# Performance work log

Measured on AMD Instinct MI355X. Metric: run time of the kernel, lower is better.

The kernel has to match this reference:

```python
import jax, jax.numpy as jnp
import numpy as np

C = 256
G = 32            # GroupNorm groups = min(32, C)
DQK = C // 8      # q/k channel dim
EPS = 1e-5


def setup_inputs() -> dict:
    key = jax.random.key(0)
    ks = jax.random.split(key, 10)
    B, H, W = 4, 64, 64
    s = 0.02
    return {
        "x": jax.random.normal(ks[0], (B, C, H, W), dtype=jnp.float32),
        "gamma": jnp.ones((C,), jnp.float32),
        "beta": jnp.zeros((C,), jnp.float32),
        "wq": jax.random.normal(ks[1], (DQK, C), jnp.float32) * s,
        "bq": jnp.zeros((DQK,), jnp.float32),
        "wk": jax.random.normal(ks[2], (DQK, C), jnp.float32) * s,
        "bk": jnp.zeros((DQK,), jnp.float32),
        "wv": jax.random.normal(ks[3], (C, C), jnp.float32) * s,
        "bv": jnp.zeros((C,), jnp.float32),
        "wp": jax.random.normal(ks[4], (C, C), jnp.float32) * s,
        "bp": jnpp if False else jnp.zeros((C,), jnp.float32),
    }


def reference(x, gamma, beta, wq, bq, wk, bk, wv, bv, wp, bp):
    B, Cc, H, W = x.shape
    N = H * W
    # GroupNorm(32, C), affine
    h = x.reshape(B, G, Cc // G, H, W)
    mu = h.mean(axis=(2, 3, 4), keepdims=True)
    var = h.var(axis=(2, 3, 4), keepdims=True)
    h = (h - mu) * jax.lax.rsqrt(var + EPS)
    h = h.reshape(B, Cc, N) * gamma[:, None] + beta[:, None]
    # 1x1 convs == per-token linear maps over channels
    q = jnp.einsum('dc,bcn->bnd', wq, h) + bq            # [B, N, DQK]
    k = jnp.einsum('dc,bcn->bdn', wk, h) + bk[:, None]   # [B, DQK, N]
    v = jnp.einsum('ec,bcn->ben', wv, h) + bv[:, None]   # [B, C, N]
    scale = DQK ** (-0.5)
    attn = jax.nn.softmax(jnp.einsum('bnd,bdm->bnm', q, k) * scale, axis=-1)
    out = jnp.einsum('bnm,bem->ben', attn, v)            # [B, C, N]
    proj = jnp.einsum('fe,ben->bfn', wp, out) + bp[:, None]
    return x + proj.reshape(B, Cc, H, W)
```

## Files before the change

### kernel.cpp

```cpp
#include <hip/hip_runtime.h>
#include <hip/hip_bf16.h>

#define NB 4
#define CD 256
#define NT 4096
#define DQ 32

typedef __attribute__((ext_vector_type(8))) __bf16 bf16x8;
typedef __attribute__((ext_vector_type(16))) float float16v;
typedef __attribute__((ext_vector_type(4))) unsigned int uint4v;
typedef __attribute__((ext_vector_type(2))) unsigned int uint2v;

#if __has_builtin(__builtin_amdgcn_exp2f)
#define EXP2(x) __builtin_amdgcn_exp2f(x)
#else
#define EXP2(x) exp2f(x)
#endif

__device__ inline unsigned short f2bf(float f) {
  unsigned u = __float_as_uint(f);
  u += 0x7fffu + ((u >> 16) & 1u);
  return (unsigned short)(u >> 16);
}

__global__ __launch_bounds__(256) void gn_prep(
    const float* __restrict__ x, float* __restrict__ accum,
    const float* __restrict__ wq, const float* __restrict__ wk,
    const float* __restrict__ wv, const float* __restrict__ wp,
    const float* __restrict__ bq, const float* __restrict__ bk,
    const float* __restrict__ bv, unsigned short* __restrict__ wqkv,
    unsigned short* __restrict__ wpb, float* __restrict__ bias) {
  int bx = blockIdx.x;
  int tid = threadIdx.x;
  if (bx < 512) {
    int bg = bx >> 2, ch = bx & 3;
    const float4* xp = (const float4*)(x + (size_t)bg * 32768 + ch * 8192);
    float s = 0.f, ss = 0.f;
#pragma unroll
    for (int i = 0; i < 8; i++) {
      float4 v = xp[tid + 256 * i];
      s += v.x + v.y + v.z + v.w;
      ss += v.x * v.x + v.y * v.y + v.z * v.z + v.w * v.w;
    }
    int wid = tid >> 6, lane = tid & 63;
#pragma unroll
    for (int off = 32; off >= 1; off >>= 1) {
      s += __shfl_xor(s, off);
      ss += __shfl_xor(ss, off);
    }
    __shared__ float red[8];
    if (lane == 0) { red[wid] = s; red[4 + wid] = ss; }
    __syncthreads();
    if (tid == 0) {
      accum[2 * bx] = red[0] + red[1] + red[2] + red[3];
      accum[2 * bx + 1] = red[4] + red[5] + red[6] + red[7];
    }
  } else {
    const float scale2 = 0.2550348909867343f;
    int i = (bx - 512) * 256 + tid;
    if (i < 320 * 256) {
      int j = i >> 8, c = i & 255;
      float v;
      if (j < 32) v = wq[j * 256 + c] * scale2;
      else if (j < 64) v = wk[(j - 32) * 256 + c];
      else v = wv[(j - 64) * 256 + c];
      wqkv[i] = f2bf(v);
    } else if (i < 320 * 256 + 256 * 256) {
      int k = i - 320 * 256;
      wpb[k] = f2bf(wp[k]);
    } else if (i < 320 * 256 + 256 * 256 + 320) {
      int j = i - (320 * 256 + 256 * 256);
      float v;
      if (j < 32) v = bq[j] * scale2;
      else if (j < 64) v = bk[j - 32];
      else v = bv[j - 64];
      bias[j] = v;
    }
  }
}

__global__ __launch_bounds__(256) void gn_apply(
    const float* __restrict__ x, const float* __restrict__ gamma,
    const float* __restrict__ beta, const float* __restrict__ accum,
    unsigned short* __restrict__ h) {
  int bg = blockIdx.x >> 2, nc = blockIdx.x & 3;
  int tid = threadIdx.x;
  float S = accum[8 * bg] + accum[8 * bg + 2] + accum[8 * bg + 4] +
            accum[8 * bg + 6];
  float SS = accum[8 * bg + 1] + accum[8 * bg + 3] + accum[8 * bg + 5] +
             accum[8 * bg + 7];
  float mu = S * (1.f / 32768.f);
  float var = SS * (1.f / 32768.f) - mu * mu;
  float rstd = rsqrtf(var + 1e-5f);
  int b = bg >> 5, g = bg & 31, c0 = g * 8;
  float gam[8], bet[8];
#pragma unroll
  for (int j = 0; j < 8; j++) { gam[j] = gamma[c0 + j]; bet[j] = beta[c0 + j]; }
  const float* xb = x + (size_t)bg * 32768;
#pragma unroll
  for (int i = 0; i < 4; i++) {
    int n = nc * 1024 + tid + 256 * i;
    unsigned short hv[8];
#pragma unroll
    for (int j = 0; j < 8; j++) {
      float y = (xb[j * NT + n] - mu) * rstd * gam[j] + bet[j];
      hv[j] = f2bf(y);
    }
    *(uint4v*)(h + ((size_t)(b * NT + n) * CD + c0)) = *(uint4v*)hv;
  }
}

__global__ __launch_bounds__(256) void qkv_gemm(
    const unsigned short* __restrict__ A, const unsigned short* __restrict__ H,
    const float* __restrict__ bias, unsigned short* __restrict__ qk,
    unsigned short* __restrict__ v) {
  int nt = blockIdx.x, mt = blockIdx.y, b = blockIdx.z;
  int tid = threadIdx.x, lane = tid & 63;
  int w = tid >> 6, mi = w & 1, ni = w >> 1;
  int l31 = lane & 31, hh = lane >> 5;
  int m_base = mt * 64 + 32 * mi;
  int n_base = nt * 128 + 64 * ni;
  const unsigned short* Arow = A + (size_t)(m_base + l31) * 256 + 8 * hh;
  const unsigned short* Hb = H + (size_t)b * NT * CD;
  const unsigned short* h0 = Hb + (size_t)(n_base + l31) * CD + 8 * hh;
  const unsigned short* h1 = h0 + (size_t)32 * CD;
  float16v acc0, acc1;
#pragma unroll
  for (int r = 0; r < 16; r++) { acc0[r] = 0.f; acc1[r] = 0.f; }
#pragma unroll
  for (int s = 0; s < 16; s++) {
    bf16x8 af = *(const bf16x8*)(Arow + 16 * s);
    bf16x8 b0 = *(const bf16x8*)(h0 + 16 * s);
    bf16x8 b1 = *(const bf16x8*)(h1 + 16 * s);
    acc0 = __builtin_amdgcn_mfma_f32_32x32x16_bf16(af, b0, acc0, 0, 0, 0);
    acc1 = __builtin_amdgcn_mfma_f32_32x32x16_bf16(af, b1, acc1, 0, 0, 0);
  }
  float bj[16];
  int jr[16];
#pragma unroll
  for (int r = 0; r < 16; r++) {
    jr[r] = m_base + (r & 3) + 8 * (r >> 2) + 4 * hh;
    bj[r] = bias[jr[r]];
  }
#pragma unroll
  for (int half = 0; half < 2; half++) {
    int n = n_base + 32 * half + l31;
#pragma unroll
    for (int r = 0; r < 16; r++) {
      float val = (half ? acc1[r] : acc0[r]) + bj[r];
      int j = jr[r];
      if (j < 64) {
        qk[((size_t)b * NT + n) * 64 + j] = f2bf(val);
      } else {
        v[((size_t)b * CD + (j - 64)) * NT + n] = f2bf(val);
      }
    }
  }
}

__global__ __launch_bounds__(512, 4) void attn_fused(
    const unsigned short* __restrict__ qk, const unsigned short* __restrict__ V,
    unsigned short* __restrict__ Pa, unsigned short* __restrict__ Pb,
    float* __restrict__ lp4) {
  int bx = blockIdx.x;
  int n0 = (bx >> 1) * 64;
  int kh = bx & 1;
  int b = blockIdx.y;
  int tid = threadIdx.x, lane = tid & 63, w = tid >> 6;
  int qi = w & 1, kj = (w >> 1) & 1, eo = w >> 2;
  int l31 = lane & 31, hh = lane >> 5;

  __shared__ unsigned short Ks[64 * 36];
  __shared__ unsigned short Vs[256 * 68];
  __shared__ unsigned short Pbuf[2 * 32 * 68];

  const unsigned short* qkb = qk + (size_t)b * NT * 64;
  const unsigned short* Vb = V + (size_t)b * CD * NT;

  int n_g = n0 + 32 * qi + l31;
  bf16x8 qfr[2];
  qfr[0] = *(const bf16x8*)&qkb[(size_t)n_g * 64 + 8 * hh];
  qfr[1] = *(const bf16x8*)&qkb[(size_t)n_g * 64 + 8 * hh + 16];

  int se = tid >> 1, smh = (tid & 1) * 32;
  int skr = tid >> 2, skc = (tid & 3) * 8;

  int mbase = kh * 2048;
  uint4v vreg[4];
  uint4v kreg;
  {
    const unsigned short* vp = &Vb[(size_t)se * NT + mbase + smh];
#pragma unroll
    for (int u = 0; u < 4; u++) vreg[u] = *(const uint4v*)(vp + 8 * u);
    if (tid < 256)
      kreg = *(const uint4v*)&qkb[(size_t)(mbase + skr) * 64 + 32 + skc];
  }

  float16v acc[2];
#pragma unroll
  for (int et = 0; et < 2; et++)
#pragma unroll
    for (int r = 0; r < 16; r++) acc[et][r] = 0.f;
  float lsum = 0.f;
  unsigned short* Prow = &Pbuf[(qi * 32 + l31) * 68];

  for (int it = 0; it < 32; it++) {
    if (tid < 256) {
      *(uint4v*)&Ks[skr * 36 + skc] = kreg;
      if (it + 1 < 32) {
        int m1 = mbase + (it + 1) * 64;
        kreg = *(const uint4v*)&qkb[(size_t)(m1 + skr) * 64 + 32 + skc];
      }
    }
    __syncthreads();

#pragma unroll
    for (int u = 0; u < 4; u++)
      *(uint4v*)&Vs[se * 68 + smh + 8 * u] = vreg[u];
    if (it + 1 < 32) {
      int m1 = mbase + (it + 1) * 64;
      const unsigned short* vp = &Vb[(size_t)se * NT + m1 + smh];
#pragma unroll
      for (int u = 0; u < 4; u++) vreg[u] = *(const uint4v*)(vp + 8 * u);
    }

    if (eo == 0) {
      float16v st;
#pragma unroll
      for (int r = 0; r < 16; r++) st[r] = 0.f;
#pragma unroll
      for (int s = 0; s < 2; s++) {
        bf16x8 af = *(const bf16x8*)&Ks[(32 * kj + l31) * 36 + 16 * s + 8 * hh];
        st = __builtin_amdgcn_mfma_f32_32x32x16_bf16(af, qfr[s], st, 0, 0, 0);
      }
#pragma unroll
      for (int rq = 0; rq < 4; rq++) {
        float e0 = EXP2(st[4 * rq + 0]);
        float e1 = EXP2(st[4 * rq + 1]);
        float e2 = EXP2(st[4 * rq + 2]);
        float e3 = EXP2(st[4 * rq + 3]);
        lsum += (e0 + e1) + (e2 + e3);
        uint2v pw;
        pw[0] = __builtin_amdgcn_perm(__float_as_uint(e1), __float_as_uint(e0),
                                      0x07060302u);
        pw[1] = __builtin_amdgcn_perm(__float_as_uint(e3), __float_as_uint(e2),
                                      0x07060302u);
        *(uint2v*)&Prow[8 * rq + 4 * hh + 32 * kj] = pw;
      }
    }
    __syncthreads();

#pragma unroll
    for (int sp = 0; sp < 4; sp++) {
      bf16x8 afr =
          *(const bf16x8*)&Pbuf[(qi * 32 + l31) * 68 + 16 * sp + 8 * hh];
#pragma unroll
      for (int et = 0; et < 2; et++) {
        int etile = 4 * eo + 2 * kj + et;
        bf16x8 bfr =
            *(const bf16x8*)&Vs[(32 * etile + l31) * 68 + 16 * sp + 8 * hh];
        acc[et] =
            __builtin_amdgcn_mfma_f32_32x32x16_bf16(afr, bfr, acc[et], 0, 0, 0);
      }
    }
  }

  if (eo == 0) {
    lsum += __shfl_xor(lsum, 32);
    if (hh == 0) {
      lp4[(size_t)((kh * 2 + kj) * NB + b) * NT + n0 + 32 * qi + l31] = lsum;
    }
  }
  unsigned short* Pout = (kh ? Pb : Pa) + (size_t)b * NT * CD;
#pragma unroll
  for (int r = 0; r < 16; r++) {
    int nl = (r & 3) + 8 * (r >> 2) + 4 * hh;
    size_t row = (size_t)(n0 + 32 * qi + nl) * CD + l31;
#pragma unroll
    for (int et = 0; et < 2; et++) {
      int etile = 4 * eo + 2 * kj + et;
      Pout[row + 32 * etile] = f2bf(acc[et][r]);
    }
  }
}

__device__ inline bf16x8 combine_frag(const unsigned short* p0,
                                      const unsigned short* p1, float inv) {
  uint4v ua = *(const uint4v*)p0;
  uint4v ub = *(const uint4v*)p1;
  uint4v r;
#pragma unroll
  for (int j = 0; j < 4; j++) {
    float lo = __uint_as_float(ua[j] << 16) + __uint_as_float(ub[j] << 16);
    float hi = __uint_as_float(ua[j] & 0xffff0000u) +
               __uint_as_float(ub[j] & 0xffff0000u);
    lo *= inv;
    hi *= inv;
    r[j] = __builtin_amdgcn_perm(__float_as_uint(hi), __float_as_uint(lo),
                                 0x07060302u);
  }
  return *(bf16x8*)&r;
}

__global__ __launch_bounds__(256) void proj_gemm(
    const unsigned short* __restrict__ Wp, const unsigned short* __restrict__ Pa,
    const unsigned short* __restrict__ Pb, const float* __restrict__ lp4,
    const float* __restrict__ bp, const float* __restrict__ x,
    float* __restrict__ out) {
  int nt = blockIdx.x, mt = blockIdx.y, b = blockIdx.z;
  int tid = threadIdx.x, lane = tid & 63;
  int w = tid >> 6, mi = w & 1, ni = w >> 1;
  int l31 = lane & 31, hh = lane >> 5;
  int m_base = mt * 64 + 32 * mi;
  int n_base = nt * 128 + 64 * ni;
  const unsigned short* Arow = Wp + (size_t)(m_base + l31) * 256 + 8 * hh;
  int nA = n_base + l31, nB = nA + 32;
  float lA = 0.f, lB = 0.f;
#pragma unroll
  for (int s4 = 0; s4 < 4; s4++) {
    lA += lp4[(size_t)(s4 * NB + b) * NT + nA];
    lB += lp4[(size_t)(s4 * NB + b) * NT + nB];
  }
  float invA = 1.f / lA, invB = 1.f / lB;
  const unsigned short* a0 = Pa + ((size_t)b * NT + nA) * CD + 8 * hh;
  const unsigned short* a1 = Pa + ((size_t)b * NT + nB) * CD + 8 * hh;
  const unsigned short* c0 = Pb + ((size_t)b * NT + nA) * CD + 8 * hh;
  const unsigned short* c1 = Pb + ((size_t)b * NT + nB) * CD + 8 * hh;
  float16v acc0, acc1;
#pragma unroll
  for (int r = 0; r < 16; r++) { acc0[r] = 0.f; acc1[r] = 0.f; }
#pragma unroll
  for (int s = 0; s < 16; s++) {
    bf16x8 af = *(const bf16x8*)(Arow + 16 * s);
    bf16x8 b0 = combine_frag(a0 + 16 * s, c0 + 16 * s, invA);
    bf16x8 b1 = combine_frag(a1 + 16 * s, c1 + 16 * s, invB);
    acc0 = __builtin_amdgcn_mfma_f32_32x32x16_bf16(af, b0, acc0, 0, 0, 0);
    acc1 = __builtin_amdgcn_mfma_f32_32x32x16_bf16(af, b1, acc1, 0, 0, 0);
  }
#pragma unroll
  for (int half = 0; half < 2; half++) {
    int n = n_base + 32 * half + l31;
#pragma unroll
    for (int r = 0; r < 16; r++) {
      int f = m_base + (r & 3) + 8 * (r >> 2) + 4 * hh;
      size_t idx = ((size_t)b * CD + f) * NT + n;
      out[idx] = x[idx] + (half ? acc1[r] : acc0[r]) + bp[f];
    }
  }
}

extern "C" void kernel_launch(void* const* d_in, const int* in_sizes, int n_in,
                              void* d_out, int out_size, void* d_ws,
                              size_t ws_size, hipStream_t stream) {
  (void)in_sizes; (void)n_in; (void)out_size; (void)ws_size;
  const float* x = (const float*)d_in[0];
  const float* gamma = (const float*)d_in[1];
  const float* beta = (const float*)d_in[2];
  const float* wq = (const float*)d_in[3];
  const float* bq = (const float*)d_in[4];
  const float* wk = (const float*)d_in[5];
  const float* bk = (const float*)d_in[6];
  const float* wv = (const float*)d_in[7];
  const float* bv = (const float*)d_in[8];
  const float* wp = (const float*)d_in[9];
  const float* bp = (const float*)d_in[10];
  float* out = (float*)d_out;

  char* ws = (char*)d_ws;
  unsigned short* h_ws = (unsigned short*)ws;
  unsigned short* qk_ws = (unsigned short*)(ws + 8388608);
  unsigned short* v_ws = (unsigned short*)(ws + 10485760);
  unsigned short* o_ws = (unsigned short*)(ws + 18874368);
  unsigned short* wqkv_b = (unsigned short*)(ws + 27262976);
  unsigned short* wp_b = (unsigned short*)(ws + 27426816);
  float* bias_q = (float*)(ws + 27557888);
  float* accum = (float*)(ws + 27559168);
  float* lp4 = (float*)(ws + 27563264);

  gn_prep<<<1090, 256, 0, stream>>>(x, accum, wq, wk, wv, wp, bq, bk, bv,
                                    wqkv_b, wp_b, bias_q);
  gn_apply<<<512, 256, 0, stream>>>(x, gamma, beta, accum, h_ws);
  dim3 gq(32, 5, NB);
  qkv_gemm<<<gq, 256, 0, stream>>>(wqkv_b, h_ws, bias_q, qk_ws, v_ws);
  dim3 ga(128, NB);
  attn_fused<<<ga, 512, 0, stream>>>(qk_ws, v_ws, h_ws, o_ws, lp4);
  dim3 gp(32, 4, NB);
  proj_gemm<<<gp, 256, 0, stream>>>(wp_b, h_ws, o_ws, lp4, bp, x, out);
}
```

Before: 192.4 us.

## Fuse GroupNorm kernels and widen attention query tile to 128 rows

```diff
diff --git a/kernel.cpp b/kernel.cpp
--- a/kernel.cpp
+++ b/kernel.cpp
@@ -23,22 +23,23 @@
   return (unsigned short)(u >> 16);
 }
 
-__global__ __launch_bounds__(256) void gn_prep(
-    const float* __restrict__ x, float* __restrict__ accum,
-    const float* __restrict__ wq, const float* __restrict__ wk,
-    const float* __restrict__ wv, const float* __restrict__ wp,
-    const float* __restrict__ bq, const float* __restrict__ bk,
-    const float* __restrict__ bv, unsigned short* __restrict__ wqkv,
+__global__ __launch_bounds__(512) void gn_pack(
+    const float* __restrict__ x, const float* __restrict__ gamma,
+    const float* __restrict__ beta, const float* __restrict__ wq,
+    const float* __restrict__ wk, const float* __restrict__ wv,
+    const float* __restrict__ wp, const float* __restrict__ bq,
+    const float* __restrict__ bk, const float* __restrict__ bv,
+    unsigned short* __restrict__ h, unsigned short* __restrict__ wqkv,
     unsigned short* __restrict__ wpb, float* __restrict__ bias) {
   int bx = blockIdx.x;
   int tid = threadIdx.x;
-  if (bx < 512) {
-    int bg = bx >> 2, ch = bx & 3;
-    const float4* xp = (const float4*)(x + (size_t)bg * 32768 + ch * 8192);
+  if (bx < 128) {
+    int bg = bx;
+    const float4* xp = (const float4*)(x + (size_t)bg * 32768);
     float s = 0.f, ss = 0.f;
 #pragma unroll
-    for (int i = 0; i < 8; i++) {
-      float4 v = xp[tid + 256 * i];
+    for (int i = 0; i < 16; i++) {
+      float4 v = xp[tid + 512 * i];
       s += v.x + v.y + v.z + v.w;
       ss += v.x * v.x + v.y * v.y + v.z * v.z + v.w * v.w;
     }
@@ -48,16 +49,43 @@
       s += __shfl_xor(s, off);
       ss += __shfl_xor(ss, off);
     }
-    __shared__ float red[8];
-    if (lane == 0) { red[wid] = s; red[4 + wid] = ss; }
+    __shared__ float red[16];
+    __shared__ float stat[2];
+    if (lane == 0) { red[wid] = s; red[8 + wid] = ss; }
     __syncthreads();
     if (tid == 0) {
-      accum[2 * bx] = red[0] + red[1] + red[2] + red[3];
-      accum[2 * bx + 1] = red[4] + red[5] + red[6] + red[7];
+      float S = 0.f, SS = 0.f;
+#pragma unroll
+      for (int j = 0; j < 8; j++) { S += red[j]; SS += red[8 + j]; }
+      float mu = S * (1.f / 32768.f);
+      float var = SS * (1.f / 32768.f) - mu * mu;
+      stat[0] = mu;
+      stat[1] = rsqrtf(var + 1e-5f);
+    }
+    __syncthreads();
+    float mu = stat[0], rstd = stat[1];
+    int b = bg >> 5, g = bg & 31, c0 = g * 8;
+    float gam[8], bet[8];
+#pragma unroll
+    for (int j = 0; j < 8; j++) {
+      gam[j] = gamma[c0 + j];
+      bet[j] = beta[c0 + j];
+    }
+    const float* xb = x + (size_t)bg * 32768;
+#pragma unroll
+    for (int i = 0; i < 8; i++) {
+      int n = 512 * i + tid;
+      unsigned short hv[8];
+#pragma unroll
+      for (int j = 0; j < 8; j++) {
+        float y = (xb[j * NT + n] - mu) * rstd * gam[j] + bet[j];
+        hv[j] = f2bf(y);
+      }
+      *(uint4v*)(h + ((size_t)(b * NT + n) * CD + c0)) = *(uint4v*)hv;
     }
   } else {
     const float scale2 = 0.2550348909867343f;
-    int i = (bx - 512) * 256 + tid;
+    int i = (bx - 128) * 512 + tid;
     if (i < 320 * 256) {
       int j = i >> 8, c = i & 255;
       float v;
@@ -79,37 +107,6 @@
   }
 }
 
-__global__ __launch_bounds__(256) void gn_apply(
-    const float* __restrict__ x, const float* __restrict__ gamma,
-    const float* __restrict__ beta, const float* __restrict__ accum,
-    unsigned short* __restrict__ h) {
-  int bg = blockIdx.x >> 2, nc = blockIdx.x & 3;
-  int tid = threadIdx.x;
-  float S = accum[8 * bg] + accum[8 * bg + 2] + accum[8 * bg + 4] +
-            accum[8 * bg + 6];
-  float SS = accum[8 * bg + 1] + accum[8 * bg + 3] + accum[8 * bg + 5] +
-             accum[8 * bg + 7];
-  float mu = S * (1.f / 32768.f);
-  float var = SS * (1.f / 32768.f) - mu * mu;
-  float rstd = rsqrtf(var + 1e-5f);
-  int b = bg >> 5, g = bg & 31, c0 = g * 8;
-  float gam[8], bet[8];
-#pragma unroll
-  for (int j = 0; j < 8; j++) { gam[j] = gamma[c0 + j]; bet[j] = beta[c0 + j]; }
-  const float* xb = x + (size_t)bg * 32768;
-#pragma unroll
-  for (int i = 0; i < 4; i++) {
-    int n = nc * 1024 + tid + 256 * i;
-    unsigned short hv[8];
-#pragma unroll
-    for (int j = 0; j < 8; j++) {
-      float y = (xb[j * NT + n] - mu) * rstd * gam[j] + bet[j];
-      hv[j] = f2bf(y);
-    }
-    *(uint4v*)(h + ((size_t)(b * NT + n) * CD + c0)) = *(uint4v*)hv;
-  }
-}
-
 __global__ __launch_bounds__(256) void qkv_gemm(
     const unsigned short* __restrict__ A, const unsigned short* __restrict__ H,
     const float* __restrict__ bias, unsigned short* __restrict__ qk,
@@ -158,34 +155,40 @@
   }
 }
 
+template <int KHN>
 __global__ __launch_bounds__(512, 4) void attn_fused(
     const unsigned short* __restrict__ qk, const unsigned short* __restrict__ V,
-    unsigned short* __restrict__ Pa, unsigned short* __restrict__ Pb,
-    float* __restrict__ lp4) {
+    unsigned short* __restrict__ P0, unsigned short* __restrict__ P1,
+    unsigned short* __restrict__ P2, unsigned short* __restrict__ P3,
+    float* __restrict__ lp) {
+  constexpr int ITERS = (NT / KHN) / 64;
   int bx = blockIdx.x;
-  int n0 = (bx >> 1) * 64;
-  int kh = bx & 1;
+  int n0 = (bx / KHN) * 128;
+  int kh = bx % KHN;
   int b = blockIdx.y;
   int tid = threadIdx.x, lane = tid & 63, w = tid >> 6;
-  int qi = w & 1, kj = (w >> 1) & 1, eo = w >> 2;
   int l31 = lane & 31, hh = lane >> 5;
+  int qs = w & 3, kj = w >> 2;
+  int qih = w & 1, epair = w >> 1;
 
   __shared__ unsigned short Ks[64 * 36];
   __shared__ unsigned short Vs[256 * 68];
-  __shared__ unsigned short Pbuf[2 * 32 * 68];
+  __shared__ unsigned short Pbuf[128 * 68];
 
   const unsigned short* qkb = qk + (size_t)b * NT * 64;
   const unsigned short* Vb = V + (size_t)b * CD * NT;
 
-  int n_g = n0 + 32 * qi + l31;
   bf16x8 qfr[2];
-  qfr[0] = *(const bf16x8*)&qkb[(size_t)n_g * 64 + 8 * hh];
-  qfr[1] = *(const bf16x8*)&qkb[(size_t)n_g * 64 + 8 * hh + 16];
+  {
+    int n_g = n0 + 32 * qs + l31;
+    qfr[0] = *(const bf16x8*)&qkb[(size_t)n_g * 64 + 8 * hh];
+    qfr[1] = *(const bf16x8*)&qkb[(size_t)n_g * 64 + 8 * hh + 16];
+  }
 
   int se = tid >> 1, smh = (tid & 1) * 32;
   int skr = tid >> 2, skc = (tid & 3) * 8;
-
-  int mbase = kh * 2048;
+  int mbase = kh * (NT / KHN);
+
   uint4v vreg[4];
   uint4v kreg;
   {
@@ -196,18 +199,19 @@
       kreg = *(const uint4v*)&qkb[(size_t)(mbase + skr) * 64 + 32 + skc];
   }
 
-  float16v acc[2];
-#pragma unroll
-  for (int et = 0; et < 2; et++)
-#pragma unroll
-    for (int r = 0; r < 16; r++) acc[et][r] = 0.f;
+  float16v acc[2][2];
+#pragma unroll
+  for (int a = 0; a < 2; a++)
+#pragma unroll
+    for (int e2 = 0; e2 < 2; e2++)
+#pragma unroll
+      for (int r = 0; r < 16; r++) acc[a][e2][r] = 0.f;
   float lsum = 0.f;
-  unsigned short* Prow = &Pbuf[(qi * 32 + l31) * 68];
-
-  for (int it = 0; it < 32; it++) {
+
+  for (int it = 0; it < ITERS; it++) {
     if (tid < 256) {
       *(uint4v*)&Ks[skr * 36 + skc] = kreg;
-      if (it + 1 < 32) {
+      if (it + 1 < ITERS) {
         int m1 = mbase + (it + 1) * 64;
         kreg = *(const uint4v*)&qkb[(size_t)(m1 + skr) * 64 + 32 + skc];
       }
@@ -217,14 +221,14 @@
 #pragma unroll
     for (int u = 0; u < 4; u++)
       *(uint4v*)&Vs[se * 68 + smh + 8 * u] = vreg[u];
-    if (it + 1 < 32) {
+    if (it + 1 < ITERS) {
       int m1 = mbase + (it + 1) * 64;
       const unsigned short* vp = &Vb[(size_t)se * NT + m1 + smh];
 #pragma unroll
       for (int u = 0; u < 4; u++) vreg[u] = *(const uint4v*)(vp + 8 * u);
     }
 
-    if (eo == 0) {
+    {
       float16v st;
 #pragma unroll
       for (int r = 0; r < 16; r++) st[r] = 0.f;
@@ -233,6 +237,7 @@
         bf16x8 af = *(const bf16x8*)&Ks[(32 * kj + l31) * 36 + 16 * s + 8 * hh];
         st = __builtin_amdgcn_mfma_f32_32x32x16_bf16(af, qfr[s], st, 0, 0, 0);
       }
+      unsigned short* Prow = &Pbuf[(32 * qs + l31) * 68 + 32 * kj];
 #pragma unroll
       for (int rq = 0; rq < 4; rq++) {
         float e0 = EXP2(st[4 * rq + 0]);
@@ -245,55 +250,63 @@
                                       0x07060302u);
         pw[1] = __builtin_amdgcn_perm(__float_as_uint(e3), __float_as_uint(e2),
                                       0x07060302u);
-        *(uint2v*)&Prow[8 * rq + 4 * hh + 32 * kj] = pw;
+        *(uint2v*)&Prow[8 * rq + 4 * hh] = pw;
       }
     }
     __syncthreads();
 
 #pragma unroll
     for (int sp = 0; sp < 4; sp++) {
-      bf16x8 afr =
-          *(const bf16x8*)&Pbuf[(qi * 32 + l31) * 68 + 16 * sp + 8 * hh];
-#pragma unroll
-      for (int et = 0; et < 2; et++) {
-        int etile = 4 * eo + 2 * kj + et;
-        bf16x8 bfr =
-            *(const bf16x8*)&Vs[(32 * etile + l31) * 68 + 16 * sp + 8 * hh];
-        acc[et] =
-            __builtin_amdgcn_mfma_f32_32x32x16_bf16(afr, bfr, acc[et], 0, 0, 0);
-      }
-    }
-  }
-
-  if (eo == 0) {
-    lsum += __shfl_xor(lsum, 32);
-    if (hh == 0) {
-      lp4[(size_t)((kh * 2 + kj) * NB + b) * NT + n0 + 32 * qi + l31] = lsum;
-    }
-  }
-  unsigned short* Pout = (kh ? Pb : Pa) + (size_t)b * NT * CD;
-#pragma unroll
-  for (int r = 0; r < 16; r++) {
-    int nl = (r & 3) + 8 * (r >> 2) + 4 * hh;
-    size_t row = (size_t)(n0 + 32 * qi + nl) * CD + l31;
-#pragma unroll
-    for (int et = 0; et < 2; et++) {
-      int etile = 4 * eo + 2 * kj + et;
-      Pout[row + 32 * etile] = f2bf(acc[et][r]);
-    }
-  }
-}
-
-__device__ inline bf16x8 combine_frag(const unsigned short* p0,
-                                      const unsigned short* p1, float inv) {
-  uint4v ua = *(const uint4v*)p0;
-  uint4v ub = *(const uint4v*)p1;
+      bf16x8 a0 =
+          *(const bf16x8*)&Pbuf[(32 * (2 * qih) + l31) * 68 + 16 * sp + 8 * hh];
+      bf16x8 a1 = *(const bf16x8*)&Pbuf[(32 * (2 * qih + 1) + l31) * 68 +
+                                        16 * sp + 8 * hh];
+      bf16x8 b0 =
+          *(const bf16x8*)&Vs[(32 * (2 * epair) + l31) * 68 + 16 * sp + 8 * hh];
+      bf16x8 b1 = *(const bf16x8*)&Vs[(32 * (2 * epair + 1) + l31) * 68 +
+                                      16 * sp + 8 * hh];
+      acc[0][0] = __builtin_amdgcn_mfma_f32_32x32x16_bf16(a0, b0, acc[0][0], 0, 0, 0);
+      acc[0][1] = __builtin_amdgcn_mfma_f32_32x32x16_bf16(a0, b1, acc[0][1], 0, 0, 0);
+      acc[1][0] = __builtin_amdgcn_mfma_f32_32x32x16_bf16(a1, b0, acc[1][0], 0, 0, 0);
+      acc[1][1] = __builtin_amdgcn_mfma_f32_32x32x16_bf16(a1, b1, acc[1][1], 0, 0, 0);
+    }
+  }
+
+  lsum += __shfl_xor(lsum, 32);
+  if (hh == 0) {
+    lp[(size_t)((kh * 2 + kj) * NB + b) * NT + n0 + 32 * qs + l31] = lsum;
+  }
+  unsigned short* Pout =
+      (kh == 0 ? P0 : kh == 1 ? P1 : kh == 2 ? P2 : P3) + (size_t)b * NT * CD;
+#pragma unroll
+  for (int a = 0; a < 2; a++) {
+#pragma unroll
+    for (int r = 0; r < 16; r++) {
+      int nl = (r & 3) + 8 * (r >> 2) + 4 * hh;
+      size_t row = (size_t)(n0 + 32 * (2 * qih + a) + nl) * CD;
+#pragma unroll
+      for (int e2 = 0; e2 < 2; e2++) {
+        Pout[row + 32 * (2 * epair + e2) + l31] = f2bf(acc[a][e2][r]);
+      }
+    }
+  }
+}
+
+template <int KHN>
+__device__ inline bf16x8 combineN(const unsigned short* const* ps, size_t off,
+                                  float inv) {
+  uint4v u[KHN];
+#pragma unroll
+  for (int k = 0; k < KHN; k++) u[k] = *(const uint4v*)(ps[k] + off);
   uint4v r;
 #pragma unroll
   for (int j = 0; j < 4; j++) {
-    float lo = __uint_as_float(ua[j] << 16) + __uint_as_float(ub[j] << 16);
-    float hi = __uint_as_float(ua[j] & 0xffff0000u) +
-               __uint_as_float(ub[j] & 0xffff0000u);
+    float lo = 0.f, hi = 0.f;
+#pragma unroll
+    for (int k = 0; k < KHN; k++) {
+      lo += __uint_as_float(u[k][j] << 16);
+      hi += __uint_as_float(u[k][j] & 0xffff0000u);
+    }
     lo *= inv;
     hi *= inv;
     r[j] = __builtin_amdgcn_perm(__float_as_uint(hi), __float_as_uint(lo),
@@ -302,9 +315,12 @@
   return *(bf16x8*)&r;
 }
 
+template <int KHN>
 __global__ __launch_bounds__(256) void proj_gemm(
-    const unsigned short* __restrict__ Wp, const unsigned short* __restrict__ Pa,
-    const unsigned short* __restrict__ Pb, const float* __restrict__ lp4,
+    const unsigned short* __restrict__ Wp, const unsigned short* __restrict__ P0,
+    const unsigned short* __restrict__ P1,
+    const unsigned short* __restrict__ P2,
+    const unsigned short* __restrict__ P3, const float* __restrict__ lp,
     const float* __restrict__ bp, const float* __restrict__ x,
     float* __restrict__ out) {
   int nt = blockIdx.x, mt = blockIdx.y, b = blockIdx.z;
@@ -317,23 +333,27 @@
   int nA = n_base + l31, nB = nA + 32;
   float lA = 0.f, lB = 0.f;
 #pragma unroll
-  for (int s4 = 0; s4 < 4; s4++) {
-    lA += lp4[(size_t)(s4 * NB + b) * NT + nA];
-    lB += lp4[(size_t)(s4 * NB + b) * NT + nB];
+  for (int s4 = 0; s4 < 2 * KHN; s4++) {
+    lA += lp[(size_t)(s4 * NB + b) * NT + nA];
+    lB += lp[(size_t)(s4 * NB + b) * NT + nB];
   }
   float invA = 1.f / lA, invB = 1.f / lB;
-  const unsigned short* a0 = Pa + ((size_t)b * NT + nA) * CD + 8 * hh;
-  const unsigned short* a1 = Pa + ((size_t)b * NT + nB) * CD + 8 * hh;
-  const unsigned short* c0 = Pb + ((size_t)b * NT + nA) * CD + 8 * hh;
-  const unsigned short* c1 = Pb + ((size_t)b * NT + nB) * CD + 8 * hh;
+  const unsigned short* psA[4];
+  const unsigned short* psB[4];
+  const unsigned short* bufs[4] = {P0, P1, P2, P3};
+#pragma unroll
+  for (int k = 0; k < KHN; k++) {
+    psA[k] = bufs[k] + ((size_t)b * NT + nA) * CD + 8 * hh;
+    psB[k] = bufs[k] + ((size_t)b * NT + nB) * CD + 8 * hh;
+  }
   float16v acc0, acc1;
 #pragma unroll
   for (int r = 0; r < 16; r++) { acc0[r] = 0.f; acc1[r] = 0.f; }
 #pragma unroll
   for (int s = 0; s < 16; s++) {
     bf16x8 af = *(const bf16x8*)(Arow + 16 * s);
-    bf16x8 b0 = combine_frag(a0 + 16 * s, c0 + 16 * s, invA);
-    bf16x8 b1 = combine_frag(a1 + 16 * s, c1 + 16 * s, invB);
+    bf16x8 b0 = combineN<KHN>(psA, (size_t)(16 * s), invA);
+    bf16x8 b1 = combineN<KHN>(psB, (size_t)(16 * s), invB);
     acc0 = __builtin_amdgcn_mfma_f32_32x32x16_bf16(af, b0, acc0, 0, 0, 0);
     acc1 = __builtin_amdgcn_mfma_f32_32x32x16_bf16(af, b1, acc1, 0, 0, 0);
   }
@@ -352,7 +372,7 @@
 extern "C" void kernel_launch(void* const* d_in, const int* in_sizes, int n_in,
                               void* d_out, int out_size, void* d_ws,
                               size_t ws_size, hipStream_t stream) {
-  (void)in_sizes; (void)n_in; (void)out_size; (void)ws_size;
+  (void)in_sizes; (void)n_in; (void)out_size;
   const float* x = (const float*)d_in[0];
   const float* gamma = (const float*)d_in[1];
   const float* beta = (const float*)d_in[2];
@@ -365,25 +385,46 @@
   const float* wp = (const float*)d_in[9];
   const float* bp = (const float*)d_in[10];
   float* out = (float*)d_out;
-
   char* ws = (char*)d_ws;
+
   unsigned short* h_ws = (unsigned short*)ws;
   unsigned short* qk_ws = (unsigned short*)(ws + 8388608);
   unsigned short* v_ws = (unsigned short*)(ws + 10485760);
-  unsigned short* o_ws = (unsigned short*)(ws + 18874368);
-  unsigned short* wqkv_b = (unsigned short*)(ws + 27262976);
-  unsigned short* wp_b = (unsigned short*)(ws + 27426816);
-  float* bias_q = (float*)(ws + 27557888);
-  float* accum = (float*)(ws + 27559168);
-  float* lp4 = (float*)(ws + 27563264);
-
-  gn_prep<<<1090, 256, 0, stream>>>(x, accum, wq, wk, wv, wp, bq, bk, bv,
-                                    wqkv_b, wp_b, bias_q);
-  gn_apply<<<512, 256, 0, stream>>>(x, gamma, beta, accum, h_ws);
+  unsigned short* P1 = (unsigned short*)(ws + 18874368);
+  unsigned short* P0 = h_ws;
+
+  bool big = ws_size >= 44863488ull;
+  unsigned short *P2, *P3, *wqkv_b, *wp_b;
+  float *bias_q, *lp;
+  if (big) {
+    P2 = (unsigned short*)(ws + 27262976);
+    P3 = (unsigned short*)(ws + 35651584);
+    wqkv_b = (unsigned short*)(ws + 44040192);
+    wp_b = (unsigned short*)(ws + 44204032);
+    bias_q = (float*)(ws + 44335104);
+    lp = (float*)(ws + 44339200);
+  } else {
+    P2 = P0;
+    P3 = P1;
+    wqkv_b = (unsigned short*)(ws + 27262976);
+    wp_b = (unsigned short*)(ws + 27426816);
+    bias_q = (float*)(ws + 27557888);
+    lp = (float*)(ws + 27559168);
+  }
+
+  gn_pack<<<417, 512, 0, stream>>>(x, gamma, beta, wq, wk, wv, wp, bq, bk, bv,
+                                   h_ws, wqkv_b, wp_b, bias_q);
   dim3 gq(32, 5, NB);
   qkv_gemm<<<gq, 256, 0, stream>>>(wqkv_b, h_ws, bias_q, qk_ws, v_ws);
-  dim3 ga(128, NB);
-  attn_fused<<<ga, 512, 0, stream>>>(qk_ws, v_ws, h_ws, o_ws, lp4);
-  dim3 gp(32, 4, NB);
-  proj_gemm<<<gp, 256, 0, stream>>>(wp_b, h_ws, o_ws, lp4, bp, x, out);
-}
+  if (big) {
+    dim3 ga(128, NB);
+    attn_fused<4><<<ga, 512, 0, stream>>>(qk_ws, v_ws, P0, P1, P2, P3, lp);
+    dim3 gp(32, 4, NB);
+    proj_gemm<4><<<gp, 256, 0, stream>>>(wp_b, P0, P1, P2, P3, lp, bp, x, out);
+  } else {
+    dim3 ga(64, NB);
+    attn_fused<2><<<ga, 512, 0, stream>>>(qk_ws, v_ws, P0, P1, P2, P3, lp);
+    dim3 gp(32, 4, NB);
+    proj_gemm<2><<<gp, 256, 0, stream>>>(wp_b, P0, P1, P2, P3, lp, bp, x, out);
+  }
+}
```

New measurement: 205.4 us. +6.7%, slower.
